# Optimization experiments

Measured on AMD Instinct MI355X. Metric: run time of the kernel, lower is better.

The kernel has to match this reference:

```python
import jax, jax.numpy as jnp
import numpy as np

B, S, D = 1024, 256, 128  # batch, seq_len, emb_dim; concat feat = 4*D = 512
H1, H2 = 256, 64          # att_hidden_size tail; att_hidden_size = [4*D, H1, H2]


def setup_inputs() -> dict:
    key = jax.random.key(0)
    ks = jax.random.split(key, 8)
    queries = jax.random.normal(ks[0], (B, D), dtype=jnp.float32)
    keys = jax.random.normal(ks[1], (B, S, D), dtype=jnp.float32)
    keys_length = jax.random.randint(ks[2], (B,), 1, S + 1)  # in [1, S]
    W1 = jax.random.normal(ks[3], (4 * D, H1), dtype=jnp.float32) * (1.0 / np.sqrt(4 * D))
    b1 = jnp.zeros((H1,), dtype=jnp.float32)
    W2 = jax.random.normal(ks[4], (H1, H2), dtype=jnp.float32) * (1.0 / np.sqrt(H1))
    b2 = jnp.zeros((H2,), dtype=jnp.float32)
    Wd = jax.random.normal(ks[5], (H2, 1), dtype=jnp.float32) * (1.0 / np.sqrt(H2))
    bd = jnp.zeros((1,), dtype=jnp.float32)
    return {"queries": queries, "keys": keys, "keys_length": keys_length,
            "W1": W1, "b1": b1, "W2": W2, "b2": b2, "Wd": Wd, "bd": bd}


def reference(queries, keys, keys_length, W1, b1, W2, b2, Wd, bd):
    # broadcast query across sequence: [B, S, D]
    q = jnp.broadcast_to(queries[:, None, :], keys.shape)
    feat = jnp.concatenate([q, keys, q - keys, q * keys], axis=-1)
    # att MLP (sigmoid after each layer, as in MLPLayers)
    h = jax.nn.sigmoid(jnp.einsum('bsf,fh->bsh', feat, W1) + b1)
    h = jax.nn.sigmoid(jnp.einsum('bsh,hk->bsk', h, W2) + b2)
    score = (jnp.einsum('bsk,ko->bso', h, Wd) + bd)[..., 0]  # [B, S]
    # mask: positions >= keys_length are invalid (mask_mat = arange(S))
    mask = jnp.arange(S)[None, :] >= keys_length[:, None]
    score = jnp.where(mask, -jnp.inf, score)  # softmax_stag=True -> -inf fill
    score = score / jnp.sqrt(jnp.float32(D))
    w = jax.nn.softmax(score, axis=1)  # [B, S]
    # return_seq_weight=False -> weighted sum over keys: [B, 1, D]
    out = jnp.einsum('bs,bsd->bd', w, keys)[:, None, :]
    return out
```

## Files before the change

kernel.cpp:

```cpp
#include <hip/hip_runtime.h>


typedef unsigned short u16;
typedef unsigned int u32;
typedef short bf16x8 __attribute__((ext_vector_type(8)));
typedef float f32x4 __attribute__((ext_vector_type(4)));

#define NBATCH 1024
#define SLEN 256
#define DD 128
#define NH1 256
#define NH2 64

#define WS_WBCT  0
#define WS_WDT   65536
#define WS_W2T   131072
#define WS_WDS   163840
#define WS_WSUM  165888
#define WS_BIAS1 296960

#define L_KBUF   0
#define L_H1     16384
#define L_SCORES 32768
#define L_BIAS   33792
#define L_B2     34816
#define L_WD     35072
#define L_WPART  35344
#define L_RED4   35856
#define L_SIZE   35920

__device__ __forceinline__ u16 f2bf_rne(float f){
  union { float f; unsigned u; } v; v.f = f;
  unsigned r = v.u + 0x7fffu + ((v.u >> 16) & 1u);
  return (u16)(r >> 16);
}
__device__ __forceinline__ u32 pack_trunc(float a, float b){
  return (__float_as_uint(a) >> 16) | (__float_as_uint(b) & 0xffff0000u);
}
__device__ __forceinline__ float b2fl(short s){
  return __uint_as_float(((u32)(u16)s) << 16);
}
__device__ __forceinline__ int swz(int byte){
  return byte ^ (((byte >> 9) & 7) << 4);
}
__device__ __forceinline__ int swzk(int byte){
  return byte ^ (((byte >> 8) & 7) << 4);
}
__device__ __forceinline__ float fsigmoid(float x){
  return __builtin_amdgcn_rcpf(1.f + __expf(-x));
}
__device__ __forceinline__ void barrier_lds(){
  asm volatile("s_waitcnt lgkmcnt(0)" ::: "memory");
  __builtin_amdgcn_s_barrier();
  __builtin_amdgcn_sched_barrier(0);
}

__global__ void prep_weights(const float* __restrict__ W1, const float* __restrict__ W2,
                             const float* __restrict__ Wd, const float* __restrict__ bd,
                             u16* __restrict__ WbcT, u16* __restrict__ WdT,
                             u16* __restrict__ W2T, float* __restrict__ WdS,
                             float* __restrict__ Wsum){
  int n = blockIdx.x;
  int k = threadIdx.x;
  if (k < DD){
    WbcT[n * DD + k] = f2bf_rne(W1[(128 + k) * NH1 + n] - W1[(256 + k) * NH1 + n]);
    WdT [n * DD + k] = f2bf_rne(W1[(384 + k) * NH1 + n]);
    Wsum[k * NH1 + n] = W1[k * NH1 + n] + W1[(256 + k) * NH1 + n];
  }
  if (n < NH2) W2T[n * 256 + k] = f2bf_rne(W2[k * NH2 + n]);
  if (n == 0 && k < NH2) WdS[k] = Wd[k];
  if (n == 0 && k == NH2) WdS[NH2] = bd[0];
}

__global__ void prep_bias(const float* __restrict__ q, const float* __restrict__ Wsum,
                          const float* __restrict__ b1, float* __restrict__ bias1){
  __shared__ float qsh[DD];
  int b = blockIdx.x, j = threadIdx.x;
  if (j < DD) qsh[j] = q[b * DD + j];
  __syncthreads();
  float acc = b1[j];
  #pragma unroll 8
  for (int d = 0; d < DD; ++d)
    acc += qsh[d] * Wsum[d * NH1 + j];
  bias1[b * NH1 + j] = acc;
}

__global__ __launch_bounds__(512, 4)
void seqatt_main(const float* __restrict__ queries, const float* __restrict__ keys,
                 const int* __restrict__ keys_length,
                 const u16* __restrict__ WbcT, const u16* __restrict__ WdT,
                 const u16* __restrict__ W2Tg,
                 const float* __restrict__ WdS, const float* __restrict__ bias1g,
                 const float* __restrict__ b2g, float* __restrict__ out)
{
  __shared__ alignas(16) char smem[L_SIZE];
  float* scores = (float*)(smem + L_SCORES);
  float* bias1s = (float*)(smem + L_BIAS);
  float* b2s    = (float*)(smem + L_B2);
  float* wds    = (float*)(smem + L_WD);
  float* wpart  = (float*)(smem + L_WPART);
  float* red4   = (float*)(smem + L_RED4);

  const int b = blockIdx.x;
  const int tid = threadIdx.x;
  const int lane = tid & 63;
  const int wave = tid >> 6;
  const int l15 = lane & 15;
  const int g   = lane >> 4;
  const int r = tid >> 4, seg = tid & 15;

  if (tid < 256) bias1s[tid] = bias1g[b * NH1 + tid];
  if (tid < 64) b2s[tid] = b2g[tid];
  if (tid < 65) wds[tid] = WdS[tid];
  const int klen = keys_length[b];
  const float* kbb = keys + (long)b * SLEN * DD;

  float4 k0, k1;
#define ISSUE(t) do { const float* p_ = kbb + (((t) << 5) + r) * DD + (seg << 3); \
    k0 = *(const float4*)p_; k1 = *(const float4*)(p_ + 4); } while (0)
#define STORE(t) do { int bb_ = (((t) & 1) << 13) + (r << 8) + (seg << 4); \
    uint4 w_; \
    w_.x = pack_trunc(k0.x, k0.y); w_.y = pack_trunc(k0.z, k0.w); \
    w_.z = pack_trunc(k1.x, k1.y); w_.w = pack_trunc(k1.z, k1.w); \
    *(uint4*)(smem + swzk(bb_)) = w_; } while (0)

  ISSUE(0);

  bf16x8 bfrag[2][4];
  {
    const float* qb = queries + b * DD;
    #pragma unroll
    for (int nt = 0; nt < 2; ++nt){
      int n = (wave << 5) + (nt << 4) + l15;
      #pragma unroll
      for (int kk = 0; kk < 4; ++kk){
        int k0i = (g << 3) + (kk << 5);
        bf16x8 bc = *(const bf16x8*)(WbcT + n * DD + k0i);
        bf16x8 wd = *(const bf16x8*)(WdT  + n * DD + k0i);
        float4 q0 = *(const float4*)(qb + k0i);
        float4 q1 = *(const float4*)(qb + k0i + 4);
        float qa[8] = {q0.x, q0.y, q0.z, q0.w, q1.x, q1.y, q1.z, q1.w};
        union { u16 s[8]; bf16x8 v; } o;
        #pragma unroll
        for (int j = 0; j < 8; ++j)
          o.s[j] = f2bf_rne(fmaf(qa[j], b2fl(wd[j]), b2fl(bc[j])));
        bfrag[nt][kk] = o.v;
      }
    }
  }
  const int sh = wave >> 2;
  const int ob = (wave & 3) << 4;
  bf16x8 w2frag[8];
  #pragma unroll
  for (int kk = 0; kk < 8; ++kk)
    w2frag[kk] = *(const bf16x8*)(W2Tg + (ob + l15) * 256 + (kk << 5) + (g << 3));

  STORE(0);
  barrier_lds();

  const f32x4 fz = {0.f, 0.f, 0.f, 0.f};

  for (int st = 0; st < 8; ++st){
    const int s0 = st << 5;
    const int kb_base = (st & 1) << 13;

    if (st < 7) ISSUE(st + 1);

    f32x4 acc[2][2];
    #pragma unroll
    for (int mt = 0; mt < 2; ++mt)
      #pragma unroll
      for (int nt = 0; nt < 2; ++nt) acc[mt][nt] = fz;
    #pragma unroll
    for (int kk = 0; kk < 4; ++kk){
      bf16x8 af[2];
      #pragma unroll
      for (int mt = 0; mt < 2; ++mt)
        af[mt] = *(const bf16x8*)(smem + swzk(kb_base + (((mt << 4) + l15) << 8) + (kk << 6) + (g << 4)));
      #pragma unroll
      for (int mt = 0; mt < 2; ++mt)
        #pragma unroll
        for (int nt = 0; nt < 2; ++nt)
          acc[mt][nt] = __builtin_amdgcn_mfma_f32_16x16x32_bf16(bfrag[nt][kk], af[mt], acc[mt][nt], 0, 0, 0);
    }

    #pragma unroll
    for (int nt = 0; nt < 2; ++nt){
      float4 bia = *(const float4*)(bias1s + (wave << 5) + (nt << 4) + (g << 2));
      #pragma unroll
      for (int mt = 0; mt < 2; ++mt){
        float v0 = fsigmoid(acc[mt][nt][0] + bia.x);
        float v1 = fsigmoid(acc[mt][nt][1] + bia.y);
        float v2 = fsigmoid(acc[mt][nt][2] + bia.z);
        float v3 = fsigmoid(acc[mt][nt][3] + bia.w);
        uint2 p; p.x = pack_trunc(v0, v1); p.y = pack_trunc(v2, v3);
        int s = (mt << 4) + l15;
        int hb = (wave << 5) + (nt << 4) + (g << 2);
        *(uint2*)(smem + swz(L_H1 + (s << 9) + (hb << 1))) = p;
      }
    }
    barrier_lds();

    f32x4 acc2 = fz;
    #pragma unroll
    for (int kk = 0; kk < 8; ++kk){
      bf16x8 a2 = *(const bf16x8*)(smem + swz(L_H1 + (((sh << 4) + l15) << 9) + (kk << 6) + (g << 4)));
      acc2 = __builtin_amdgcn_mfma_f32_16x16x32_bf16(w2frag[kk], a2, acc2, 0, 0, 0);
    }

    {
      float pp = 0.f;
      #pragma unroll
      for (int i = 0; i < 4; ++i){
        int o = ob + (g << 2) + i;
        pp += fsigmoid(acc2[i] + b2s[o]) * wds[o];
      }
      pp += __shfl_xor(pp, 16); pp += __shfl_xor(pp, 32);
      if (lane < 16)
        wpart[((wave & 3) << 5) + (sh << 4) + l15] = pp;
    }

    if (st < 7) STORE(st + 1);

    barrier_lds();

    if (tid < 32){
      float v = wpart[tid] + wpart[32 + tid] + wpart[64 + tid] + wpart[96 + tid];
      int s = s0 + tid;
      scores[s] = (s < klen) ? (v + wds[64]) * 0.08838834764831845f : -1e30f;
    }
  }

  barrier_lds();

  {
    float v = (tid < 256) ? scores[tid] : -1e30f;
    float m = v;
    #pragma unroll
    for (int off = 32; off >= 1; off >>= 1) m = fmaxf(m, __shfl_xor(m, off));
    if (lane == 0) red4[wave] = m;
    __syncthreads();
    float mx = red4[0];
    #pragma unroll
    for (int w = 1; w < 8; ++w) mx = fmaxf(mx, red4[w]);
    float e = (tid < 256) ? __expf(v - mx) : 0.f;
    float ssum = e;
    #pragma unroll
    for (int off = 32; off >= 1; off >>= 1) ssum += __shfl_xor(ssum, off);
    if (lane == 0) red4[8 + wave] = ssum;
    __syncthreads();
    float tot = 0.f;
    #pragma unroll
    for (int w = 0; w < 8; ++w) tot += red4[8 + w];
    if (tid < 256) scores[tid] = e * __builtin_amdgcn_rcpf(tot);
    __syncthreads();
  }

  {
    float* red = (float*)smem;
    int d = tid & 127, q4 = tid >> 7;
    const float* kb = keys + ((long)b * SLEN + q4 * 64) * DD + d;
    const float* sc = scores + q4 * 64;
    float acc = 0.f;
    #pragma unroll 4
    for (int s2 = 0; s2 < 64; ++s2) acc += sc[s2] * kb[s2 * DD];
    red[tid] = acc;
    __syncthreads();
    if (tid < 128)
      out[b * DD + tid] = (red[tid] + red[128 + tid]) + (red[256 + tid] + red[384 + tid]);
  }
#undef ISSUE
#undef STORE
}

extern "C" void kernel_launch(void* const* d_in, const int* in_sizes, int n_in,
                              void* d_out, int out_size, void* d_ws, size_t ws_size,
                              hipStream_t stream) {
  const float* queries     = (const float*)d_in[0];
  const float* keys        = (const float*)d_in[1];
  const int*   keys_length = (const int*)d_in[2];
  const float* W1 = (const float*)d_in[3];
  const float* b1 = (const float*)d_in[4];
  const float* W2 = (const float*)d_in[5];
  const float* b2 = (const float*)d_in[6];
  const float* Wd = (const float*)d_in[7];
  const float* bd = (const float*)d_in[8];
  float* out = (float*)d_out;
  char* ws = (char*)d_ws;

  u16*   WbcT  = (u16*)(ws + WS_WBCT);
  u16*   WdT   = (u16*)(ws + WS_WDT);
  u16*   W2T   = (u16*)(ws + WS_W2T);
  float* WdS   = (float*)(ws + WS_WDS);
  float* Wsum  = (float*)(ws + WS_WSUM);
  float* bias1 = (float*)(ws + WS_BIAS1);

  prep_weights<<<dim3(256), dim3(256), 0, stream>>>(W1, W2, Wd, bd, WbcT, WdT, W2T, WdS, Wsum);
  prep_bias<<<dim3(NBATCH), dim3(256), 0, stream>>>(queries, Wsum, b1, bias1);
  seqatt_main<<<dim3(NBATCH), dim3(512), 0, stream>>>(queries, keys, keys_length,
                                                      WbcT, WdT, W2T, WdS, bias1, b2, out);
}
```

Measured before the change: 89.55 us.

## Fuse per-batch bias precompute into main kernel and split W2 MFMA chain

```diff
diff --git a/kernel.cpp b/kernel.cpp
--- a/kernel.cpp
+++ b/kernel.cpp
@@ -17,7 +17,6 @@
 #define WS_W2T   131072
 #define WS_WDS   163840
 #define WS_WSUM  165888
-#define WS_BIAS1 296960
 
 #define L_KBUF   0
 #define L_H1     16384
@@ -72,25 +71,13 @@
   if (n == 0 && k == NH2) WdS[NH2] = bd[0];
 }
 
-__global__ void prep_bias(const float* __restrict__ q, const float* __restrict__ Wsum,
-                          const float* __restrict__ b1, float* __restrict__ bias1){
-  __shared__ float qsh[DD];
-  int b = blockIdx.x, j = threadIdx.x;
-  if (j < DD) qsh[j] = q[b * DD + j];
-  __syncthreads();
-  float acc = b1[j];
-  #pragma unroll 8
-  for (int d = 0; d < DD; ++d)
-    acc += qsh[d] * Wsum[d * NH1 + j];
-  bias1[b * NH1 + j] = acc;
-}
-
 __global__ __launch_bounds__(512, 4)
 void seqatt_main(const float* __restrict__ queries, const float* __restrict__ keys,
                  const int* __restrict__ keys_length,
                  const u16* __restrict__ WbcT, const u16* __restrict__ WdT,
                  const u16* __restrict__ W2Tg,
-                 const float* __restrict__ WdS, const float* __restrict__ bias1g,
+                 const float* __restrict__ WdS, const float* __restrict__ Wsum,
+                 const float* __restrict__ b1g,
                  const float* __restrict__ b2g, float* __restrict__ out)
 {
   __shared__ alignas(16) char smem[L_SIZE];
@@ -109,7 +96,6 @@
   const int g   = lane >> 4;
   const int r = tid >> 4, seg = tid & 15;
 
-  if (tid < 256) bias1s[tid] = bias1g[b * NH1 + tid];
   if (tid < 64) b2s[tid] = b2g[tid];
   if (tid < 65) wds[tid] = WdS[tid];
   const int klen = keys_length[b];
@@ -125,6 +111,20 @@
     *(uint4*)(smem + swzk(bb_)) = w_; } while (0)
 
   ISSUE(0);
+
+  {
+    float* qsh  = scores;
+    float* part = (float*)(smem + 8192);
+    if (tid < 128) qsh[tid] = queries[b * DD + tid];
+    barrier_lds();
+    int j = tid & 255, hf = tid >> 8;
+    const float* wp = Wsum + (hf << 6) * NH1 + j;
+    const float* qp = qsh + (hf << 6);
+    float acc = hf ? 0.f : b1g[j];
+    #pragma unroll 8
+    for (int d = 0; d < 64; ++d) acc = fmaf(qp[d], wp[d * NH1], acc);
+    part[(hf << 8) + j] = acc;
+  }
 
   bf16x8 bfrag[2][4];
   {
@@ -155,6 +155,12 @@
   for (int kk = 0; kk < 8; ++kk)
     w2frag[kk] = *(const bf16x8*)(W2Tg + (ob + l15) * 256 + (kk << 5) + (g << 3));
 
+  barrier_lds();
+  if (tid < 256){
+    const float* part = (const float*)(smem + 8192);
+    bias1s[tid] = part[tid] + part[256 + tid];
+  }
+
   STORE(0);
   barrier_lds();
 
@@ -201,11 +207,16 @@
     }
     barrier_lds();
 
-    f32x4 acc2 = fz;
-    #pragma unroll
-    for (int kk = 0; kk < 8; ++kk){
+    f32x4 acc2a = fz, acc2b = fz;
+    #pragma unroll
+    for (int kk = 0; kk < 4; ++kk){
       bf16x8 a2 = *(const bf16x8*)(smem + swz(L_H1 + (((sh << 4) + l15) << 9) + (kk << 6) + (g << 4)));
-      acc2 = __builtin_amdgcn_mfma_f32_16x16x32_bf16(w2frag[kk], a2, acc2, 0, 0, 0);
+      acc2a = __builtin_amdgcn_mfma_f32_16x16x32_bf16(w2frag[kk], a2, acc2a, 0, 0, 0);
+    }
+    #pragma unroll
+    for (int kk = 4; kk < 8; ++kk){
+      bf16x8 a2 = *(const bf16x8*)(smem + swz(L_H1 + (((sh << 4) + l15) << 9) + (kk << 6) + (g << 4)));
+      acc2b = __builtin_amdgcn_mfma_f32_16x16x32_bf16(w2frag[kk], a2, acc2b, 0, 0, 0);
     }
 
     {
@@ -213,7 +224,7 @@
       #pragma unroll
       for (int i = 0; i < 4; ++i){
         int o = ob + (g << 2) + i;
-        pp += fsigmoid(acc2[i] + b2s[o]) * wds[o];
+        pp += fsigmoid((acc2a[i] + acc2b[i]) + b2s[o]) * wds[o];
       }
       pp += __shfl_xor(pp, 16); pp += __shfl_xor(pp, 32);
       if (lane < 16)
@@ -293,10 +304,8 @@
   u16*   W2T   = (u16*)(ws + WS_W2T);
   float* WdS   = (float*)(ws + WS_WDS);
   float* Wsum  = (float*)(ws + WS_WSUM);
-  float* bias1 = (float*)(ws + WS_BIAS1);
 
   prep_weights<<<dim3(256), dim3(256), 0, stream>>>(W1, W2, Wd, bd, WbcT, WdT, W2T, WdS, Wsum);
-  prep_bias<<<dim3(NBATCH), dim3(256), 0, stream>>>(queries, Wsum, b1, bias1);
   seqatt_main<<<dim3(NBATCH), dim3(512), 0, stream>>>(queries, keys, keys_length,
-                                                      WbcT, WdT, W2T, WdS, bias1, b2, out);
-}
+                                                      WbcT, WdT, W2T, WdS, Wsum, b1, b2, out);
+}
```

Result: slower. 97.90 us (+9.3%).

## Process 64 sequence rows per stage instead of 32 to halve barriers

Applied to the files above, without the earlier changes.

```diff
diff --git a/kernel.cpp b/kernel.cpp
--- a/kernel.cpp
+++ b/kernel.cpp
@@ -20,14 +20,14 @@
 #define WS_BIAS1 296960
 
 #define L_KBUF   0
-#define L_H1     16384
-#define L_SCORES 32768
-#define L_BIAS   33792
-#define L_B2     34816
-#define L_WD     35072
-#define L_WPART  35344
-#define L_RED4   35856
-#define L_SIZE   35920
+#define L_H1     32768
+#define L_SCORES 65536
+#define L_BIAS   66560
+#define L_B2     67584
+#define L_WD     67840
+#define L_WPART  68112
+#define L_RED4   69136
+#define L_SIZE   69200
 
 __device__ __forceinline__ u16 f2bf_rne(float f){
   union { float f; unsigned u; } v; v.f = f;
@@ -107,7 +107,7 @@
   const int wave = tid >> 6;
   const int l15 = lane & 15;
   const int g   = lane >> 4;
-  const int r = tid >> 4, seg = tid & 15;
+  const int r = tid >> 3, seg = tid & 7;
 
   if (tid < 256) bias1s[tid] = bias1g[b * NH1 + tid];
   if (tid < 64) b2s[tid] = b2g[tid];
@@ -115,14 +115,18 @@
   const int klen = keys_length[b];
   const float* kbb = keys + (long)b * SLEN * DD;
 
-  float4 k0, k1;
-#define ISSUE(t) do { const float* p_ = kbb + (((t) << 5) + r) * DD + (seg << 3); \
-    k0 = *(const float4*)p_; k1 = *(const float4*)(p_ + 4); } while (0)
-#define STORE(t) do { int bb_ = (((t) & 1) << 13) + (r << 8) + (seg << 4); \
+  float4 k0, k1, k2, k3;
+#define ISSUE(t) do { const float* p_ = kbb + (((t) << 6) + r) * DD + (seg << 4); \
+    k0 = *(const float4*)p_;       k1 = *(const float4*)(p_ + 4); \
+    k2 = *(const float4*)(p_ + 8); k3 = *(const float4*)(p_ + 12); } while (0)
+#define STORE(t) do { int bb_ = (((t) & 1) << 14) + (r << 8) + (seg << 5); \
     uint4 w_; \
     w_.x = pack_trunc(k0.x, k0.y); w_.y = pack_trunc(k0.z, k0.w); \
     w_.z = pack_trunc(k1.x, k1.y); w_.w = pack_trunc(k1.z, k1.w); \
-    *(uint4*)(smem + swzk(bb_)) = w_; } while (0)
+    *(uint4*)(smem + swzk(bb_)) = w_; \
+    w_.x = pack_trunc(k2.x, k2.y); w_.y = pack_trunc(k2.z, k2.w); \
+    w_.z = pack_trunc(k3.x, k3.y); w_.w = pack_trunc(k3.z, k3.w); \
+    *(uint4*)(smem + swzk(bb_ + 16)) = w_; } while (0)
 
   ISSUE(0);
 
@@ -148,7 +152,7 @@
       }
     }
   }
-  const int sh = wave >> 2;
+  const int shh = wave >> 2;
   const int ob = (wave & 3) << 4;
   bf16x8 w2frag[8];
   #pragma unroll
@@ -160,72 +164,85 @@
 
   const f32x4 fz = {0.f, 0.f, 0.f, 0.f};
 
-  for (int st = 0; st < 8; ++st){
-    const int s0 = st << 5;
-    const int kb_base = (st & 1) << 13;
-
-    if (st < 7) ISSUE(st + 1);
-
-    f32x4 acc[2][2];
-    #pragma unroll
-    for (int mt = 0; mt < 2; ++mt)
-      #pragma unroll
-      for (int nt = 0; nt < 2; ++nt) acc[mt][nt] = fz;
-    #pragma unroll
-    for (int kk = 0; kk < 4; ++kk){
-      bf16x8 af[2];
+  for (int st = 0; st < 4; ++st){
+    const int s0 = st << 6;
+    const int kb_base = (st & 1) << 14;
+
+    if (st < 3) ISSUE(st + 1);
+
+    #pragma unroll
+    for (int mc = 0; mc < 2; ++mc){
+      f32x4 acc[2][2];
       #pragma unroll
       for (int mt = 0; mt < 2; ++mt)
-        af[mt] = *(const bf16x8*)(smem + swzk(kb_base + (((mt << 4) + l15) << 8) + (kk << 6) + (g << 4)));
+        #pragma unroll
+        for (int nt = 0; nt < 2; ++nt) acc[mt][nt] = fz;
+      #pragma unroll
+      for (int kk = 0; kk < 4; ++kk){
+        bf16x8 af[2];
+        #pragma unroll
+        for (int mt = 0; mt < 2; ++mt)
+          af[mt] = *(const bf16x8*)(smem + swzk(kb_base + (((mc << 5) + (mt << 4) + l15) << 8) + (kk << 6) + (g << 4)));
+        #pragma unroll
+        for (int mt = 0; mt < 2; ++mt)
+          #pragma unroll
+          for (int nt = 0; nt < 2; ++nt)
+            acc[mt][nt] = __builtin_amdgcn_mfma_f32_16x16x32_bf16(bfrag[nt][kk], af[mt], acc[mt][nt], 0, 0, 0);
+      }
+      #pragma unroll
+      for (int nt = 0; nt < 2; ++nt){
+        float4 bia = *(const float4*)(bias1s + (wave << 5) + (nt << 4) + (g << 2));
+        #pragma unroll
+        for (int mt = 0; mt < 2; ++mt){
+          float v0 = fsigmoid(acc[mt][nt][0] + bia.x);
+          float v1 = fsigmoid(acc[mt][nt][1] + bia.y);
+          float v2 = fsigmoid(acc[mt][nt][2] + bia.z);
+          float v3 = fsigmoid(acc[mt][nt][3] + bia.w);
+          uint2 p; p.x = pack_trunc(v0, v1); p.y = pack_trunc(v2, v3);
+          int s = (mc << 5) + (mt << 4) + l15;
+          int hb = (wave << 5) + (nt << 4) + (g << 2);
+          *(uint2*)(smem + swz(L_H1 + (s << 9) + (hb << 1))) = p;
+        }
+      }
+    }
+    barrier_lds();
+
+    f32x4 acc2[2];
+    acc2[0] = fz; acc2[1] = fz;
+    #pragma unroll
+    for (int kk = 0; kk < 8; ++kk){
+      bf16x8 a2[2];
       #pragma unroll
       for (int mt = 0; mt < 2; ++mt)
-        #pragma unroll
-        for (int nt = 0; nt < 2; ++nt)
-          acc[mt][nt] = __builtin_amdgcn_mfma_f32_16x16x32_bf16(bfrag[nt][kk], af[mt], acc[mt][nt], 0, 0, 0);
-    }
-
-    #pragma unroll
-    for (int nt = 0; nt < 2; ++nt){
-      float4 bia = *(const float4*)(bias1s + (wave << 5) + (nt << 4) + (g << 2));
-      #pragma unroll
-      for (int mt = 0; mt < 2; ++mt){
-        float v0 = fsigmoid(acc[mt][nt][0] + bia.x);
-        float v1 = fsigmoid(acc[mt][nt][1] + bia.y);
-        float v2 = fsigmoid(acc[mt][nt][2] + bia.z);
-        float v3 = fsigmoid(acc[mt][nt][3] + bia.w);
-        uint2 p; p.x = pack_trunc(v0, v1); p.y = pack_trunc(v2, v3);
-        int s = (mt << 4) + l15;
-        int hb = (wave << 5) + (nt << 4) + (g << 2);
-        *(uint2*)(smem + swz(L_H1 + (s << 9) + (hb << 1))) = p;
-      }
-    }
-    barrier_lds();
-
-    f32x4 acc2 = fz;
-    #pragma unroll
-    for (int kk = 0; kk < 8; ++kk){
-      bf16x8 a2 = *(const bf16x8*)(smem + swz(L_H1 + (((sh << 4) + l15) << 9) + (kk << 6) + (g << 4)));
-      acc2 = __builtin_amdgcn_mfma_f32_16x16x32_bf16(w2frag[kk], a2, acc2, 0, 0, 0);
+        a2[mt] = *(const bf16x8*)(smem + swz(L_H1 + (((shh << 5) + (mt << 4) + l15) << 9) + (kk << 6) + (g << 4)));
+      #pragma unroll
+      for (int mt = 0; mt < 2; ++mt)
+        acc2[mt] = __builtin_amdgcn_mfma_f32_16x16x32_bf16(w2frag[kk], a2[mt], acc2[mt], 0, 0, 0);
     }
 
     {
-      float pp = 0.f;
+      float pp0 = 0.f, pp1 = 0.f;
       #pragma unroll
       for (int i = 0; i < 4; ++i){
         int o = ob + (g << 2) + i;
-        pp += fsigmoid(acc2[i] + b2s[o]) * wds[o];
-      }
-      pp += __shfl_xor(pp, 16); pp += __shfl_xor(pp, 32);
-      if (lane < 16)
-        wpart[((wave & 3) << 5) + (sh << 4) + l15] = pp;
-    }
-
-    if (st < 7) STORE(st + 1);
+        float b2v = b2s[o], wdv = wds[o];
+        pp0 += fsigmoid(acc2[0][i] + b2v) * wdv;
+        pp1 += fsigmoid(acc2[1][i] + b2v) * wdv;
+      }
+      pp0 += __shfl_xor(pp0, 16); pp0 += __shfl_xor(pp0, 32);
+      pp1 += __shfl_xor(pp1, 16); pp1 += __shfl_xor(pp1, 32);
+      if (lane < 16){
+        wpart[((wave & 3) << 6) + (shh << 5) + l15]      = pp0;
+        wpart[((wave & 3) << 6) + (shh << 5) + 16 + l15] = pp1;
+      }
+    }
+
+    if (st < 3) STORE(st + 1);
 
     barrier_lds();
 
-    if (tid < 32){
-      float v = wpart[tid] + wpart[32 + tid] + wpart[64 + tid] + wpart[96 + tid];
+    if (tid < 64){
+      float v = wpart[tid] + wpart[64 + tid] + wpart[128 + tid] + wpart[192 + tid];
       int s = s0 + tid;
       scores[s] = (s < klen) ? (v + wds[64]) * 0.08838834764831845f : -1e30f;
     }
```

New measurement: 140.9 us. +57.3%, slower.
